# Optimization experiments

Measured on AMD Instinct MI355X. Metric: run time of the kernel, lower is better.

Reference implementation:

```python
import jax, jax.numpy as jnp
import numpy as np

B, N = 128, 128            # pairs, max nodes per subgraph
E, T, R = 64, 32, 32       # entity_dim, type_dim, relation_dim
NODE_SIZE, TYPE_NUM, REL_NUM = 400000, 200, 50


def _lin(k, fi, fo):
    lim = 1.0 / np.sqrt(fi)
    kw, kb = jax.random.split(k)
    W = jax.random.uniform(kw, (fi, fo), jnp.float32, -lim, lim)
    b = jax.random.uniform(kb, (fo,), jnp.float32, -lim, lim)
    return W, b


def setup_inputs() -> dict:
    key = jax.random.key(0)
    ks = jax.random.split(key, 20)
    inp = {}
    inp['node_slice'] = jax.random.randint(ks[0], (B, N), 0, NODE_SIZE + 1)
    inp['type_slice'] = jax.random.randint(ks[1], (B, N), 0, TYPE_NUM + 1)
    inp['distance_slice'] = jax.random.uniform(ks[2], (B, N), jnp.float32, 1.0, 5.0)
    inp['rel_matrix'] = jax.random.randint(ks[3], (B, N, N), 0, REL_NUM + 1)  # 0 == no edge
    inp['input_length'] = jax.random.randint(ks[4], (B,), N // 2, N + 1)
    inp['isBatch'] = 1
    inp['emb_table'] = jax.random.normal(ks[5], (NODE_SIZE + 1, E), jnp.float32) * 0.02
    inp['type_table'] = jax.random.normal(ks[6], (TYPE_NUM + 1, T), jnp.float32) * 0.02
    inp['rel_table'] = jax.random.normal(ks[7], (REL_NUM + 1, R), jnp.float32) * 0.02
    inp['W_in'], inp['b_in'] = _lin(ks[8], E + R, E)
    gi = (T + E) + E  # propogator: cat(now_input, hidden)
    inp['Wr'], inp['br'] = _lin(ks[9], gi, E)
    inp['Wz'], inp['bz'] = _lin(ks[10], gi, E)
    inp['Wt'], inp['bt'] = _lin(ks[11], gi, E)
    inp['W_co'], inp['b_co'] = _lin(ks[12], 2 * E, E)
    inp['W1'], inp['b1'] = _lin(ks[13], 3 * E, 128)
    inp['W2'], inp['b2'] = _lin(ks[14], 128, 64)
    inp['W3'], inp['b3'] = _lin(ks[15], 64, 32)
    inp['W4'], inp['b4'] = _lin(ks[16], 32, 1)
    return inp


def _ggnn(node_slice, type_slice, distance_slice, rel_matrix, input_length,
          emb_table, type_table, rel_table, W_in, b_in, Wr, br, Wz, bz, Wt, bt,
          W_co, b_co, W1, b1, W2, b2, W3, b3, W4, b4):
    node_emb = emb_table[node_slice]    # [B,N,E]
    type_emb = type_table[type_slice]   # [B,N,T]
    hidden0 = jax.lax.stop_gradient(node_emb)  # torch: .clone().detach()
    discount = (-0.1 * distance_slice)[..., None]              # [B,N,1]
    len_mask = jnp.arange(N)[None, :] < input_length[:, None]  # [B,N]
    neg = -jnp.inf

    def step(hidden, i):
        rel_vec = jax.lax.dynamic_index_in_dim(rel_matrix, i, axis=1, keepdims=False)  # [B,N]
        valid = (rel_vec != 0) & len_mask                       # nonzero relation & real node
        rel_emb = rel_table[rel_vec]                            # [B,N,R]
        pre = jax.nn.relu(jnp.concatenate([hidden, rel_emb], -1) @ W_in + b_in)  # [B,N,E]
        scaled = pre * discount
        dis_pre = jnp.max(jnp.where(valid[..., None], scaled, neg), axis=1)      # [B,E]
        dis_pre = jnp.where(valid.any(axis=1)[:, None], dis_pre, 0.0)
        now_in = jnp.concatenate([
            jax.lax.dynamic_index_in_dim(type_emb, i, axis=1, keepdims=False),
            jax.lax.dynamic_index_in_dim(node_emb, i, axis=1, keepdims=False)], -1)  # [B,T+E]
        a = jnp.concatenate([now_in, dis_pre], -1)
        r = jax.nn.sigmoid(a @ Wr + br)
        z = jax.nn.sigmoid(a @ Wz + bz)
        h_hat = jnp.tanh(jnp.concatenate([now_in, r * dis_pre], -1) @ Wt + bt)
        upd = (1.0 - z) * dis_pre + z * h_hat                   # [B,E]
        active = (i < input_length)[:, None]
        old = jax.lax.dynamic_index_in_dim(hidden, i, axis=1, keepdims=False)
        new_row = jnp.where(active, upd, old)
        hidden = jax.lax.dynamic_update_index_in_dim(hidden, new_row, i, axis=1)
        return hidden, None

    hidden, _ = jax.lax.scan(step, hidden0, jnp.arange(N))

    user = hidden[:, 0]                                          # [B,E]
    item = jnp.take_along_axis(hidden, (input_length - 1)[:, None, None], axis=1)[:, 0]
    sub = jnp.max(jnp.where(len_mask[..., None], hidden, neg), axis=1)  # [B,E]
    ua = jax.nn.relu(jnp.concatenate([user, sub], -1) @ W_co + b_co)
    ia = jax.nn.relu(jnp.concatenate([item, sub], -1) @ W_co + b_co)
    temp = jnp.concatenate([ua * user, sub, ia * item], -1)      # [B,3E]
    h = jax.nn.relu(temp @ W1 + b1)
    h = jax.nn.relu(h @ W2 + b2)
    h = jax.nn.relu(h @ W3 + b3)
    out = h @ W4 + b4                                            # [B,1]
    return jax.nn.sigmoid(out)[:, 0]                             # [B]


def reference(node_slice, type_slice, distance_slice, rel_matrix, input_length, isBatch,
              emb_table, type_table, rel_table, W_in, b_in, Wr, br, Wz, bz, Wt, bt,
              W_co, b_co, W1, b1, W2, b2, W3, b3, W4, b4):
    # batch path (isBatch=True) of GGNN.forward
    return _ggnn(node_slice, type_slice, distance_slice, rel_matrix, input_length,
                 emb_table, type_table, rel_table, W_in, b_in, Wr, br, Wz, bz, Wt, bt,
                 W_co, b_co, W1, b1, W2, b2, W3, b3, W4, b4)
```

## Files before the change

### kernel.cpp

```cpp
#include <hip/hip_runtime.h>
#include <hip/hip_bf16.h>


#define B_ 128
#define N_ 128

typedef unsigned short u16;
typedef unsigned int u32;

__device__ __forceinline__ float b2f(u16 u) {
    union { u32 i; float f; } c; c.i = ((u32)u) << 16; return c.f;
}
__device__ __forceinline__ u16 f2b(float f) {
    union { float f; u32 i; } c; c.f = f;
    u32 u = c.i;
    return (u16)((u + 0x7fffu + ((u >> 16) & 1u)) >> 16);
}
__device__ __forceinline__ float sigmoidf_(float x) { return 1.0f / (1.0f + __expf(-x)); }
__device__ __forceinline__ float tanhf_(float x) { return 1.0f - 2.0f / (__expf(2.0f * x) + 1.0f); }
__device__ __forceinline__ float rlane(float v, int k) {
    return __int_as_float(__builtin_amdgcn_readlane(__float_as_int(v), k));
}
#define BARRIER() asm volatile("s_waitcnt lgkmcnt(0)\n\ts_barrier" ::: "memory")

__device__ __forceinline__ void combine_write(float mA, float mB, int e,
                                              float* __restrict__ slotbase)
{
    int s0 = (e >> 1) << 2, s1 = ((e >> 1) + 32) << 2;
    float v0a = __int_as_float(__builtin_amdgcn_ds_bpermute(s0, __float_as_int(mA)));
    float v0b = __int_as_float(__builtin_amdgcn_ds_bpermute(s0, __float_as_int(mB)));
    float v1a = __int_as_float(__builtin_amdgcn_ds_bpermute(s1, __float_as_int(mA)));
    float v1b = __int_as_float(__builtin_amdgcn_ds_bpermute(s1, __float_as_int(mB)));
    float c0 = (e & 1) ? v0b : v0a;
    float c1 = (e & 1) ? v1b : v1a;
    slotbase[e] = fmaxf(c0, c1);
}

template<int NJ>
__device__ __forceinline__ void bloop(
    int b, int w, int e, int p, int half, int len,
    const float* __restrict__ Hws,
    const unsigned char* __restrict__ relL,
    const u32* __restrict__ relW32,
    const float* __restrict__ disc,
    float* __restrict__ pmaxF,
    const float* __restrict__ updH)
{
    const float NEGINF = -__builtin_inff();
    const int base = w * 48 + half * NJ;

    float hA[NJ], hB[NJ], dreg[NJ];
    {
        const float2* H2 = (const float2*)(Hws + (size_t)b * N_ * 64);
        #pragma unroll
        for (int jj = 0; jj < NJ; ++jj) {
            float2 v = H2[(base + jj) * 32 + p];
            hA[jj] = v.x; hB[jj] = v.y;
            dreg[jj] = disc[base + jj];
        }
    }

    {
        float mA = NEGINF, mB = NEGINF;
        const u32* rw = (const u32*)(relL + base);
        #pragma unroll
        for (int g = 0; g < NJ / 4; ++g) {
            u32 d = rw[g];
            #pragma unroll
            for (int bb = 0; bb < 4; ++bb) {
                const int jj = 4 * g + bb;
                u32 rr = (d >> (bb * 8)) & 255u;
                u32 pr = relW32[(rr << 5) + p];
                float rwbA = __uint_as_float(pr << 16);
                float rwbB = __uint_as_float(pr & 0xffff0000u);
                float dd = dreg[jj];
                float sA = fmaxf(hA[jj] + rwbA, 0.f) * dd;
                float sB = fmaxf(hB[jj] + rwbB, 0.f) * dd;
                mA = rr ? fmaxf(mA, sA) : mA;
                mB = rr ? fmaxf(mB, sB) : mB;
            }
        }
        combine_write(mA, mB, e, pmaxF + (w << 6));
    }
    BARRIER();

    for (int i = 0; i < len; ++i) {
        if (i > 0) {
            const int prev = i - 1;
            const int ow = (prev < 48) ? 0 : (prev < 96) ? 1 : 2;
            if (w == ow) {
                float2 u = ((const float2*)updH)[p];
                const int off = prev - ow * 48;
                const int hs = off / NJ;
                const int oj = off % NJ;
                if (half == hs) {
                    #pragma unroll
                    for (int jj = 0; jj < NJ; ++jj) if (jj == oj) {
                        hA[jj] = u.x; hB[jj] = u.y;
                    }
                }
            }
        }
        if (i + 1 < len) {
            float mA = NEGINF, mB = NEGINF;
            const u32* rw = (const u32*)(relL + (i + 1) * N_ + base);
            const int sl = i - base;
            #pragma unroll
            for (int g = 0; g < NJ / 4; ++g) {
                u32 d = rw[g];
                #pragma unroll
                for (int bb = 0; bb < 4; ++bb) {
                    const int jj = 4 * g + bb;
                    u32 rr = (d >> (bb * 8)) & 255u;
                    rr = (jj == sl) ? 0u : rr;
                    u32 pr = relW32[(rr << 5) + p];
                    float rwbA = __uint_as_float(pr << 16);
                    float rwbB = __uint_as_float(pr & 0xffff0000u);
                    float dd = dreg[jj];
                    float sA = fmaxf(hA[jj] + rwbA, 0.f) * dd;
                    float sB = fmaxf(hB[jj] + rwbB, 0.f) * dd;
                    mA = rr ? fmaxf(mA, sA) : mA;
                    mB = rr ? fmaxf(mB, sB) : mB;
                }
            }
            combine_write(mA, mB, e, pmaxF + ((i & 1) ^ 1) * 192 + (w << 6));
        }
        BARRIER();
    }
}

__global__ __launch_bounds__(256, 2) void ggnn_pre(
    const int* __restrict__ node_slice, const int* __restrict__ type_slice,
    const float* __restrict__ emb_table, const float* __restrict__ type_table,
    const float* __restrict__ W_in,
    const float* __restrict__ Wr, const float* __restrict__ br,
    const float* __restrict__ Wz, const float* __restrict__ bz,
    const float* __restrict__ Wt, const float* __restrict__ bt,
    u16* __restrict__ NTbf, float* __restrict__ Hws)
{
    const int b  = blockIdx.x >> 4;
    const int i0 = (blockIdx.x & 15) * 8;
    const int t = threadIdx.x;
    const int w = t >> 6;
    const int e = t & 63;

    float wc[96];
    float bias = 0.f;
    if (w < 3) {
        const float* W  = (w == 0) ? Wr : (w == 1) ? Wz : Wt;
        const float* bb = (w == 0) ? br : (w == 1) ? bz : bt;
        bias = bb[e];
        #pragma unroll
        for (int k = 0; k < 96; ++k) wc[k] = W[k * 64 + e];
    } else {
        #pragma unroll
        for (int k = 0; k < 64; ++k) wc[k] = W_in[k * 64 + e];
        #pragma unroll
        for (int k = 64; k < 96; ++k) wc[k] = 0.f;
    }

    int nodes[8], typs[8];
    #pragma unroll
    for (int r = 0; r < 8; ++r) {
        nodes[r] = node_slice[b * N_ + i0 + r];
        typs[r]  = type_slice[b * N_ + i0 + r];
    }

    float xa[8], xb[8];
    #pragma unroll
    for (int r = 0; r < 8; ++r) {
        const float* pa = (e < 32)
            ? (type_table + (size_t)typs[r] * 32 + e)
            : (emb_table + (size_t)nodes[r] * 64 + (e - 32));
        xa[r] = *pa;
        xb[r] = emb_table[(size_t)nodes[r] * 64 + 32 + (e & 31)];
    }

    #pragma unroll
    for (int r = 0; r < 8; ++r) {
        if (w < 3) {
            float a0 = bias, a1 = 0.f, a2 = 0.f, a3 = 0.f;
            #pragma unroll
            for (int k = 0; k < 32; k += 4) {
                a0 += rlane(xa[r], k)     * wc[k];
                a1 += rlane(xa[r], k + 1) * wc[k + 1];
                a2 += rlane(xa[r], k + 2) * wc[k + 2];
                a3 += rlane(xa[r], k + 3) * wc[k + 3];
            }
            #pragma unroll
            for (int k = 0; k < 32; k += 4) {
                a0 += rlane(xa[r], 32 + k)     * wc[32 + k];
                a1 += rlane(xa[r], 32 + k + 1) * wc[32 + k + 1];
                a2 += rlane(xa[r], 32 + k + 2) * wc[32 + k + 2];
                a3 += rlane(xa[r], 32 + k + 3) * wc[32 + k + 3];
            }
            #pragma unroll
            for (int k = 32; k < 64; k += 4) {
                a0 += rlane(xb[r], k - 32) * wc[32 + k];
                a1 += rlane(xb[r], k - 31) * wc[32 + k + 1];
                a2 += rlane(xb[r], k - 30) * wc[32 + k + 2];
                a3 += rlane(xb[r], k - 29) * wc[32 + k + 3];
            }
            NTbf[(size_t)(b * N_ + i0 + r) * 192 + w * 64 + e] =
                f2b((a0 + a1) + (a2 + a3));
        } else {
            float a0 = 0.f, a1 = 0.f, a2 = 0.f, a3 = 0.f;
            #pragma unroll
            for (int k = 0; k < 32; k += 4) {
                a0 += rlane(xa[r], 32 + k)     * wc[k];
                a1 += rlane(xa[r], 32 + k + 1) * wc[k + 1];
                a2 += rlane(xa[r], 32 + k + 2) * wc[k + 2];
                a3 += rlane(xa[r], 32 + k + 3) * wc[k + 3];
            }
            #pragma unroll
            for (int k = 32; k < 64; k += 4) {
                a0 += rlane(xb[r], k - 32) * wc[k];
                a1 += rlane(xb[r], k - 31) * wc[k + 1];
                a2 += rlane(xb[r], k - 30) * wc[k + 2];
                a3 += rlane(xb[r], k - 29) * wc[k + 3];
            }
            Hws[(size_t)(b * N_ + i0 + r) * 64 + e] = (a0 + a1) + (a2 + a3);
        }
    }
}

__global__ __launch_bounds__(256, 1) void ggnn_main(
    const int* __restrict__ rel_matrix,
    const int* __restrict__ input_length, const float* __restrict__ distance,
    const float* __restrict__ rel_table,
    const float* __restrict__ W_in, const float* __restrict__ b_in,
    const float* __restrict__ Wr, const float* __restrict__ Wz, const float* __restrict__ Wt,
    const float* __restrict__ W_co, const float* __restrict__ b_co,
    const float* __restrict__ W1, const float* __restrict__ b1,
    const float* __restrict__ W2, const float* __restrict__ b2,
    const float* __restrict__ W3, const float* __restrict__ b3,
    const float* __restrict__ W4, const float* __restrict__ b4,
    const u16* __restrict__ NTbf, const float* __restrict__ Hws,
    float* __restrict__ out)
{
    __shared__ __align__(16) u32   relW32[51 * 32];
    __shared__ __align__(16) unsigned char relL[128 * 128];
    __shared__ __align__(16) float disc[N_];
    __shared__ __align__(16) float pmaxF[2 * 192];
    __shared__ __align__(16) float updH[64];
    __shared__ __align__(16) float userrow[64], itemrow[64], submrow[64];
    __shared__ __align__(16) float temp[192];
    __shared__ float h1[128];
    __shared__ float h2v[64];
    __shared__ float h3v[32];

    const int b = blockIdx.x;
    const int t = threadIdx.x;
    const int w = t >> 6;
    const int e = t & 63;
    const int p = e & 31;
    const int half = e >> 5;
    const int len = input_length[b];
    const float NEGINF = -__builtin_inff();

    if (t < N_) disc[t] = -0.1f * distance[b * N_ + t];

    {
        const int4* src = (const int4*)(rel_matrix + b * N_ * N_);
        u32* dst = (u32*)relL;
        for (int c = t; c < 4096; c += 256) {
            int4 v = src[c];
            int j = (c * 4) & 127;
            u32 pk = (u32)((j + 0 < len && v.x) ? v.x : 0)
                   | ((u32)((j + 1 < len && v.y) ? v.y : 0) << 8)
                   | ((u32)((j + 2 < len && v.z) ? v.z : 0) << 16)
                   | ((u32)((j + 3 < len && v.w) ? v.w : 0) << 24);
            dst[c] = pk;
        }
    }
    for (int idx = t; idx < 51 * 32; idx += 256) {
        int r = idx >> 5, pp = idx & 31;
        float aA = b_in[2 * pp], aB = b_in[2 * pp + 1];
        #pragma unroll
        for (int k = 0; k < 32; ++k) {
            float rt = rel_table[r * 32 + k];
            aA += rt * W_in[(64 + k) * 64 + 2 * pp];
            aB += rt * W_in[(64 + k) * 64 + 2 * pp + 1];
        }
        relW32[idx] = (u32)f2b(aA) | ((u32)f2b(aB) << 16);
    }
    __syncthreads();

    if (w < 3) {
        if (w == 2) bloop<16>(b, w, e, p, half, len, Hws, relL, relW32,
                              disc, pmaxF, updH);
        else        bloop<24>(b, w, e, p, half, len, Hws, relL, relW32,
                              disc, pmaxF, updH);
    } else {
        float wcr[64], wcz[64], wct[64], wcH[64];
        #pragma unroll
        for (int k = 0; k < 64; ++k) {
            wcr[k] = Wr[(96 + k) * 64 + e];
            wcz[k] = Wz[(96 + k) * 64 + e];
            wct[k] = Wt[(96 + k) * 64 + e];
            wcH[k] = W_in[k * 64 + e];
        }
        const u16* NTb = NTbf + (size_t)b * N_ * 192;
        u16 ncr = NTb[e], ncz = NTb[64 + e], nct = NTb[128 + e];
        float uH = 0.f;
        float user_r = 0.f, item_r = 0.f, subm_r = NEGINF;
        BARRIER();

        for (int i = 0; i < len; ++i) {
            const float* pm = pmaxF + (i & 1) * 192;
            float mm = fmaxf(fmaxf(pm[e], pm[64 + e]), pm[128 + e]);
            if (i > 0) {
                int rb = relL[i * N_ + (i - 1)];
                if (rb) {
                    u32 pr = relW32[(rb << 5) + (e >> 1)];
                    float rwb = __uint_as_float((e & 1) ? (pr & 0xffff0000u)
                                                        : (pr << 16));
                    mm = fmaxf(mm, fmaxf(uH + rwb, 0.f) * disc[i - 1]);
                }
            }
            float dis0 = (mm == NEGINF) ? 0.f : mm;

            const int nrow = ((i + 1) & 127) * 192;
            u16 npr = NTb[nrow + e], npz = NTb[nrow + 64 + e],
                npt = NTb[nrow + 128 + e];

            float ra0 = b2f(ncr), ra1 = 0.f, ra2 = 0.f, ra3 = 0.f;
            float za0 = b2f(ncz), za1 = 0.f, za2 = 0.f, za3 = 0.f;
            #pragma unroll
            for (int k = 0; k < 64; k += 4) {
                float s0 = rlane(dis0, k),     s1 = rlane(dis0, k + 1);
                float s2 = rlane(dis0, k + 2), s3 = rlane(dis0, k + 3);
                ra0 += s0 * wcr[k];     za0 += s0 * wcz[k];
                ra1 += s1 * wcr[k + 1]; za1 += s1 * wcz[k + 1];
                ra2 += s2 * wcr[k + 2]; za2 += s2 * wcz[k + 2];
                ra3 += s3 * wcr[k + 3]; za3 += s3 * wcz[k + 3];
            }
            float r = sigmoidf_((ra0 + ra1) + (ra2 + ra3));
            float z = sigmoidf_((za0 + za1) + (za2 + za3));
            float rdp = r * dis0;

            float ta0 = b2f(nct), ta1 = 0.f, ta2 = 0.f, ta3 = 0.f;
            #pragma unroll
            for (int k = 0; k < 64; k += 4) {
                ta0 += rlane(rdp, k)     * wct[k];
                ta1 += rlane(rdp, k + 1) * wct[k + 1];
                ta2 += rlane(rdp, k + 2) * wct[k + 2];
                ta3 += rlane(rdp, k + 3) * wct[k + 3];
            }
            float hh = tanhf_((ta0 + ta1) + (ta2 + ta3));
            float upd = (1.f - z) * dis0 + z * hh;
            if (i == 0) user_r = upd;
            subm_r = fmaxf(subm_r, upd);
            item_r = upd;

            float ha0 = 0.f, ha1 = 0.f, ha2 = 0.f, ha3 = 0.f;
            #pragma unroll
            for (int k = 0; k < 64; k += 4) {
                ha0 += rlane(upd, k)     * wcH[k];
                ha1 += rlane(upd, k + 1) * wcH[k + 1];
                ha2 += rlane(upd, k + 2) * wcH[k + 2];
                ha3 += rlane(upd, k + 3) * wcH[k + 3];
            }
            uH = (ha0 + ha1) + (ha2 + ha3);
            updH[e] = uH;
            ncr = npr; ncz = npz; nct = npt;
            BARRIER();
        }
        userrow[e] = user_r; itemrow[e] = item_r; submrow[e] = subm_r;
    }
    __syncthreads();

    if (t < 128) {
        const int half2 = t >> 6;
        const float* row = (half2 == 0) ? userrow : itemrow;
        float acc = b_co[e];
        #pragma unroll
        for (int k = 0; k < 64; ++k) acc += row[k] * W_co[k * 64 + e];
        #pragma unroll
        for (int k = 0; k < 64; ++k) acc += submrow[k] * W_co[(64 + k) * 64 + e];
        float act = fmaxf(acc, 0.f);
        temp[half2 * 128 + e] = act * row[e];
    } else if (t < 192) {
        temp[64 + (t - 128)] = submrow[t - 128];
    }
    __syncthreads();

    if (t < 128) {
        float acc = b1[t];
        for (int k = 0; k < 192; ++k) acc += temp[k] * W1[k * 128 + t];
        h1[t] = fmaxf(acc, 0.f);
    }
    __syncthreads();
    if (t < 64) {
        float acc = b2[t];
        for (int k = 0; k < 128; ++k) acc += h1[k] * W2[k * 64 + t];
        h2v[t] = fmaxf(acc, 0.f);
    }
    __syncthreads();
    if (t < 32) {
        float acc = b3[t];
        for (int k = 0; k < 64; ++k) acc += h2v[k] * W3[k * 32 + t];
        h3v[t] = fmaxf(acc, 0.f);
    }
    __syncthreads();
    if (t == 0) {
        float acc = b4[0];
        for (int k = 0; k < 32; ++k) acc += h3v[k] * W4[k];
        out[b] = sigmoidf_(acc);
    }
}

extern "C" void kernel_launch(void* const* d_in, const int* in_sizes, int n_in,
                              void* d_out, int out_size, void* d_ws, size_t ws_size,
                              hipStream_t stream)
{
    const int*   node_slice = (const int*)d_in[0];
    const int*   type_slice = (const int*)d_in[1];
    const float* distance   = (const float*)d_in[2];
    const int*   rel_matrix = (const int*)d_in[3];
    const int*   input_len  = (const int*)d_in[4];
    const float* emb_table  = (const float*)d_in[6];
    const float* type_table = (const float*)d_in[7];
    const float* rel_table  = (const float*)d_in[8];
    const float* W_in = (const float*)d_in[9];  const float* b_in = (const float*)d_in[10];
    const float* Wr   = (const float*)d_in[11]; const float* br   = (const float*)d_in[12];
    const float* Wz   = (const float*)d_in[13]; const float* bz   = (const float*)d_in[14];
    const float* Wt   = (const float*)d_in[15]; const float* bt   = (const float*)d_in[16];
    const float* W_co = (const float*)d_in[17]; const float* b_co = (const float*)d_in[18];
    const float* W1   = (const float*)d_in[19]; const float* b1   = (const float*)d_in[20];
    const float* W2   = (const float*)d_in[21]; const float* b2   = (const float*)d_in[22];
    const float* W3   = (const float*)d_in[23]; const float* b3   = (const float*)d_in[24];
    const float* W4   = (const float*)d_in[25]; const float* b4   = (const float*)d_in[26];

    u16*   NTbf = (u16*)d_ws;
    float* Hws  = (float*)((char*)d_ws + (size_t)B_ * N_ * 192 * 2);

    ggnn_pre<<<dim3(2048), dim3(256), 0, stream>>>(
        node_slice, type_slice, emb_table, type_table,
        W_in, Wr, br, Wz, bz, Wt, bt, NTbf, Hws);

    ggnn_main<<<dim3(B_), dim3(256), 0, stream>>>(
        rel_matrix, input_len, distance, rel_table,
        W_in, b_in, Wr, Wz, Wt, W_co, b_co,
        W1, b1, W2, b2, W3, b3, W4, b4,
        NTbf, Hws, (float*)d_out);
}
```

Measured before the change: 377.8 us.

## Move Wt/W_in GRU weights to LDS and make the no-edge case branchless via a sentinel

Moves the Wt and W_in columns for the serial GRU wave out of registers into LDS, packed as float4 tiles, and reads them each step. This cuts register pressure from four 64-float arrays to two. It also replaces the per-edge `rr ? max : skip` select with a sentinel relation entry (row 0 set to bf16 -inf) so that absent edges contribute -inf, and removes the subdiagonal mask by zeroing those entries in LDS and handling them from a precomputed sub_l array. The added LDS reads on the critical serial path may add latency, and the sentinel trick relies on -inf propagating correctly through relu*discount.

```diff
diff --git a/kernel.cpp b/kernel.cpp
--- a/kernel.cpp
+++ b/kernel.cpp
@@ -74,10 +74,8 @@
                 float rwbA = __uint_as_float(pr << 16);
                 float rwbB = __uint_as_float(pr & 0xffff0000u);
                 float dd = dreg[jj];
-                float sA = fmaxf(hA[jj] + rwbA, 0.f) * dd;
-                float sB = fmaxf(hB[jj] + rwbB, 0.f) * dd;
-                mA = rr ? fmaxf(mA, sA) : mA;
-                mB = rr ? fmaxf(mB, sB) : mB;
+                mA = fmaxf(mA, fmaxf(hA[jj] + rwbA, 0.f) * dd);
+                mB = fmaxf(mB, fmaxf(hB[jj] + rwbB, 0.f) * dd);
             }
         }
         combine_write(mA, mB, e, pmaxF + (w << 6));
@@ -91,8 +89,8 @@
             if (w == ow) {
                 float2 u = ((const float2*)updH)[p];
                 const int off = prev - ow * 48;
-                const int hs = off / NJ;
-                const int oj = off % NJ;
+                const int hs = (off >= NJ) ? 1 : 0;
+                const int oj = off - hs * NJ;
                 if (half == hs) {
                     #pragma unroll
                     for (int jj = 0; jj < NJ; ++jj) if (jj == oj) {
@@ -104,7 +102,6 @@
         if (i + 1 < len) {
             float mA = NEGINF, mB = NEGINF;
             const u32* rw = (const u32*)(relL + (i + 1) * N_ + base);
-            const int sl = i - base;
             #pragma unroll
             for (int g = 0; g < NJ / 4; ++g) {
                 u32 d = rw[g];
@@ -112,15 +109,12 @@
                 for (int bb = 0; bb < 4; ++bb) {
                     const int jj = 4 * g + bb;
                     u32 rr = (d >> (bb * 8)) & 255u;
-                    rr = (jj == sl) ? 0u : rr;
                     u32 pr = relW32[(rr << 5) + p];
                     float rwbA = __uint_as_float(pr << 16);
                     float rwbB = __uint_as_float(pr & 0xffff0000u);
                     float dd = dreg[jj];
-                    float sA = fmaxf(hA[jj] + rwbA, 0.f) * dd;
-                    float sB = fmaxf(hB[jj] + rwbB, 0.f) * dd;
-                    mA = rr ? fmaxf(mA, sA) : mA;
-                    mB = rr ? fmaxf(mB, sB) : mB;
+                    mA = fmaxf(mA, fmaxf(hA[jj] + rwbA, 0.f) * dd);
+                    mB = fmaxf(mB, fmaxf(hB[jj] + rwbB, 0.f) * dd);
                 }
             }
             combine_write(mA, mB, e, pmaxF + ((i & 1) ^ 1) * 192 + (w << 6));
@@ -241,8 +235,10 @@
     __shared__ __align__(16) u32   relW32[51 * 32];
     __shared__ __align__(16) unsigned char relL[128 * 128];
     __shared__ __align__(16) float disc[N_];
+    __shared__ __align__(16) u32   sub_l[128];
     __shared__ __align__(16) float pmaxF[2 * 192];
     __shared__ __align__(16) float updH[64];
+    __shared__ __align__(16) float4 wTH[2 * 16 * 64];
     __shared__ __align__(16) float userrow[64], itemrow[64], submrow[64];
     __shared__ __align__(16) float temp[192];
     __shared__ float h1[128];
@@ -284,6 +280,27 @@
         }
         relW32[idx] = (u32)f2b(aA) | ((u32)f2b(aB) << 16);
     }
+    {
+        float* wf = (float*)wTH;
+        for (int idx = t; idx < 8192; idx += 256) {
+            int tbl = idx >> 12;
+            int rem = idx & 4095;
+            int kc  = rem >> 8;
+            int ee  = (rem >> 2) & 63;
+            int d   = idx & 3;
+            int k   = kc * 4 + d;
+            wf[idx] = tbl ? W_in[k * 64 + ee] : Wt[(96 + k) * 64 + ee];
+        }
+    }
+    __syncthreads();
+
+    if (t < 127) {
+        u32 v = relL[(t + 1) * N_ + t];
+        sub_l[t] = v;
+        relL[(t + 1) * N_ + t] = 0;
+    }
+    if (t == 127) sub_l[127] = 0;
+    if (t < 32) relW32[t] = 0x7f807f80u;
     __syncthreads();
 
     if (w < 3) {
@@ -292,33 +309,36 @@
         else        bloop<24>(b, w, e, p, half, len, Hws, relL, relW32,
                               disc, pmaxF, updH);
     } else {
-        float wcr[64], wcz[64], wct[64], wcH[64];
+        float wcr[64], wcz[64];
         #pragma unroll
         for (int k = 0; k < 64; ++k) {
             wcr[k] = Wr[(96 + k) * 64 + e];
             wcz[k] = Wz[(96 + k) * 64 + e];
-            wct[k] = Wt[(96 + k) * 64 + e];
-            wcH[k] = W_in[k * 64 + e];
-        }
+        }
+        const float4* wtL = wTH + e;
+        const float4* whL = wTH + 1024 + e;
+
         const u16* NTb = NTbf + (size_t)b * N_ * 192;
         u16 ncr = NTb[e], ncz = NTb[64 + e], nct = NTb[128 + e];
         float uH = 0.f;
         float user_r = 0.f, item_r = 0.f, subm_r = NEGINF;
+        u32 prn = 0x7f807f80u;
+        float ddn = -1.0f;
         BARRIER();
 
         for (int i = 0; i < len; ++i) {
             const float* pm = pmaxF + (i & 1) * 192;
             float mm = fmaxf(fmaxf(pm[e], pm[64 + e]), pm[128 + e]);
-            if (i > 0) {
-                int rb = relL[i * N_ + (i - 1)];
-                if (rb) {
-                    u32 pr = relW32[(rb << 5) + (e >> 1)];
-                    float rwb = __uint_as_float((e & 1) ? (pr & 0xffff0000u)
-                                                        : (pr << 16));
-                    mm = fmaxf(mm, fmaxf(uH + rwb, 0.f) * disc[i - 1]);
-                }
+            {
+                float rwb = __uint_as_float((e & 1) ? (prn & 0xffff0000u)
+                                                    : (prn << 16));
+                mm = fmaxf(mm, fmaxf(uH + rwb, 0.f) * ddn);
             }
             float dis0 = (mm == NEGINF) ? 0.f : mm;
+
+            u32 rb2 = sub_l[i];
+            u32 pr2 = relW32[(rb2 << 5) + (e >> 1)];
+            float dd2 = disc[i];
 
             const int nrow = ((i + 1) & 127) * 192;
             u16 npr = NTb[nrow + e], npz = NTb[nrow + 64 + e],
@@ -341,11 +361,12 @@
 
             float ta0 = b2f(nct), ta1 = 0.f, ta2 = 0.f, ta3 = 0.f;
             #pragma unroll
-            for (int k = 0; k < 64; k += 4) {
-                ta0 += rlane(rdp, k)     * wct[k];
-                ta1 += rlane(rdp, k + 1) * wct[k + 1];
-                ta2 += rlane(rdp, k + 2) * wct[k + 2];
-                ta3 += rlane(rdp, k + 3) * wct[k + 3];
+            for (int kc = 0; kc < 16; ++kc) {
+                float4 wv = wtL[kc * 64];
+                float s0 = rlane(rdp, 4 * kc),     s1 = rlane(rdp, 4 * kc + 1);
+                float s2 = rlane(rdp, 4 * kc + 2), s3 = rlane(rdp, 4 * kc + 3);
+                ta0 += s0 * wv.x; ta1 += s1 * wv.y;
+                ta2 += s2 * wv.z; ta3 += s3 * wv.w;
             }
             float hh = tanhf_((ta0 + ta1) + (ta2 + ta3));
             float upd = (1.f - z) * dis0 + z * hh;
@@ -355,15 +376,18 @@
 
             float ha0 = 0.f, ha1 = 0.f, ha2 = 0.f, ha3 = 0.f;
             #pragma unroll
-            for (int k = 0; k < 64; k += 4) {
-                ha0 += rlane(upd, k)     * wcH[k];
-                ha1 += rlane(upd, k + 1) * wcH[k + 1];
-                ha2 += rlane(upd, k + 2) * wcH[k + 2];
-                ha3 += rlane(upd, k + 3) * wcH[k + 3];
+            for (int kc = 0; kc < 16; ++kc) {
+                float4 wv = whL[kc * 64];
+                float s0 = rlane(upd, 4 * kc),     s1 = rlane(upd, 4 * kc + 1);
+                float s2 = rlane(upd, 4 * kc + 2), s3 = rlane(upd, 4 * kc + 3);
+                ha0 += s0 * wv.x; ha1 += s1 * wv.y;
+                ha2 += s2 * wv.z; ha3 += s3 * wv.w;
             }
             uH = (ha0 + ha1) + (ha2 + ha3);
             updH[e] = uH;
+
             ncr = npr; ncz = npz; nct = npt;
+            prn = pr2; ddn = dd2;
             BARRIER();
         }
         userrow[e] = user_r; itemrow[e] = item_r; submrow[e] = subm_r;
```

Measured after the change: 365.6 us. 3.2% less time.
